# Kernel optimization log

Hardware: AMD Instinct MI355X
Metric: run time of the kernel (lower is better)

Reference implementation:

```python
import jax, jax.numpy as jnp
import numpy as np

ALPHA = 0.2  # LeakyReLU negative slope
NEG_BIG = -9e15

def setup_inputs() -> dict:
    key = jax.random.key(0)
    k1, k2, k3, k4 = jax.random.split(key, 4)
    B, N, Fin, Fout = 32, 1024, 64, 64
    x = jax.random.normal(k1, (B, N, Fin), dtype=jnp.float32)
    adj = jax.random.randint(k2, (B, N, N), 0, 2, dtype=jnp.int32)
    W = jax.random.normal(k3, (Fin, Fout), dtype=jnp.float32) * (1.414 / np.sqrt(Fin))
    a = jax.random.normal(k4, (2 * Fout, 1), dtype=jnp.float32) * 0.1
    return {"x": x, "adj": adj, "W": W, "a": a}

def reference(x, adj, W, a):
    # x: [B,N,Fin], adj: [B,N,N], W: [Fin,Fout], a: [2*Fout,1]
    h = jnp.einsum('bnf,fo->bno', x, W)               # [B,N,Fout]
    Fout = W.shape[1]
    a1 = a[:Fout, 0]                                   # source half
    a2 = a[Fout:, 0]                                   # target half
    # e_ij = leakyrelu(a1.h_i + a2.h_j)  (equivalent to concat+matmul)
    f = h @ a1                                         # [B,N]
    g = h @ a2                                         # [B,N]
    e = jax.nn.leaky_relu(f[:, :, None] + g[:, None, :], ALPHA)  # [B,N,N]
    att = jnp.where(adj > 0, e, jnp.float32(NEG_BIG))
    att = jax.nn.softmax(att, axis=2)                  # dropout p=0, eval mode
    h_prime = jnp.einsum('bij,bjo->bio', att, h)       # [B,N,Fout]
    return jax.nn.elu(h_prime)                         # concat=True -> elu
```

## Files before the change

### kernel.cpp

```cpp
#include <hip/hip_runtime.h>
#include <hip/hip_bf16.h>
#include <hip/hip_fp16.h>

#define NN 1024
#define FD 64
#define BB 32

typedef __attribute__((ext_vector_type(4))) float    f32x4;
typedef __attribute__((ext_vector_type(8))) _Float16 f16x8;

static __device__ __forceinline__ unsigned short f2hu(float x) {
  _Float16 h = (_Float16)x;
  return __builtin_bit_cast(unsigned short, h);
}

__global__ __launch_bounds__(256) void gat_k1(
    const float* __restrict__ x, const float* __restrict__ W,
    const float* __restrict__ av, float* __restrict__ fv,
    float* __restrict__ gv, unsigned short* __restrict__ hT)
{
  __shared__ __align__(16) float Wl[FD * FD];
  __shared__ __align__(16) float xl[FD * 68];
  __shared__ __align__(16) unsigned short tl[FD * FD];
  __shared__ __align__(16) float al[2 * FD];

  const int tid = threadIdx.x;
  const int b   = blockIdx.x >> 4;
  const int n0  = (blockIdx.x & 15) << 6;

  if (tid < 32) ((f32x4*)al)[tid] = ((const f32x4*)av)[tid];
  {
    const int r  = tid >> 2;
    const int cb = (tid & 3) << 2;
    const f32x4* Wg = (const f32x4*)W;
    const f32x4* xg = (const f32x4*)(x + ((size_t)(b * NN + n0)) * FD);
#pragma unroll
    for (int k = 0; k < 4; ++k) {
      f32x4 wv = Wg[r * 16 + cb + k];
      f32x4 xv = xg[r * 16 + cb + k];
      *(f32x4*)(Wl + r * FD + ((cb + k) << 2)) = wv;
      *(f32x4*)(xl + r * 68 + ((cb + k) << 2)) = xv;
    }
  }
  __syncthreads();

  const int r  = tid >> 2;
  const int o0 = (tid & 3) << 4;
  float acc[16];
#pragma unroll
  for (int i = 0; i < 16; ++i) acc[i] = 0.f;

#pragma unroll 8
  for (int f = 0; f < FD; ++f) {
    float xv = xl[r * 68 + f];
    const f32x4* wr = (const f32x4*)(Wl + f * FD + o0);
#pragma unroll
    for (int c = 0; c < 4; ++c) {
      f32x4 wv = wr[c];
      acc[c * 4 + 0] += xv * wv.x;
      acc[c * 4 + 1] += xv * wv.y;
      acc[c * 4 + 2] += xv * wv.z;
      acc[c * 4 + 3] += xv * wv.w;
    }
  }

  float fp = 0.f, gp = 0.f;
#pragma unroll
  for (int i = 0; i < 16; ++i) {
    fp += acc[i] * al[o0 + i];
    gp += acc[i] * al[FD + o0 + i];
  }
  fp += __shfl_xor(fp, 1); fp += __shfl_xor(fp, 2);
  gp += __shfl_xor(gp, 1); gp += __shfl_xor(gp, 2);
  if ((tid & 3) == 0) {
    fv[b * NN + n0 + r] = fp;
    gv[b * NN + n0 + r] = gp;
  }

#pragma unroll
  for (int i = 0; i < 16; ++i) {
    int o  = o0 + i;
    int sw = (o ^ (o >> 3)) & 7;
    tl[o * FD + ((((r >> 3) ^ sw) << 3) | (r & 7))] = f2hu(acc[i]);
  }
  __syncthreads();
  {
    const int c2 = tid & 7;
#pragma unroll
    for (int hh = 0; hh < 2; ++hh) {
      int o  = (tid >> 3) + 32 * hh;
      int sw = (o ^ (o >> 3)) & 7;
      f32x4 v = *(const f32x4*)(tl + o * FD + ((c2 ^ sw) << 3));
      *(f32x4*)(hT + ((size_t)(b * FD + o)) * NN + n0 + c2 * 8) = v;
    }
  }
}

__global__ __launch_bounds__(256) void gat_k2(
    const int* __restrict__ adj, const float* __restrict__ fv,
    const float* __restrict__ gv, const unsigned short* __restrict__ hT,
    float* __restrict__ out)
{
  __shared__ __align__(16) unsigned short Pl[2][32 * 64];
  __shared__ __align__(16) unsigned short Hl[2][64 * 64];
  __shared__ __align__(16) float gl[NN];
  __shared__ float dLds[32];
  __shared__ float red[8];

  const int tid  = threadIdx.x;
  const int b    = blockIdx.x >> 5;
  const int i0   = (blockIdx.x & 31) << 5;
  const int st   = blockIdx.x & 15;
  const int lane = tid & 63, w = tid >> 6;
  const int q = tid >> 3, s = tid & 7;
  const int bN = b * NN;

  f32x4 g4 = *(const f32x4*)(gv + bN + tid * 4);
  *(f32x4*)(gl + tid * 4) = g4;
  float gm = fmaxf(fmaxf(g4.x, g4.y), fmaxf(g4.z, g4.w));
  float fm = fv[bN + i0 + (tid & 31)];
#pragma unroll
  for (int m = 1; m < 64; m <<= 1) {
    gm = fmaxf(gm, __shfl_xor(gm, m));
    fm = fmaxf(fm, __shfl_xor(fm, m));
  }
  if (lane == 0) { red[w * 2] = gm; red[w * 2 + 1] = fm; }
  const float fr = fv[bN + i0 + q];
  __syncthreads();
  gm = fmaxf(fmaxf(red[0], red[2]), fmaxf(red[4], red[6]));
  fm = fmaxf(fmaxf(red[1], red[3]), fmaxf(red[5], red[7]));
  const float sm = fm + gm;
  const float Cb = fmaxf(sm, 0.2f * sm);

  const int*            adjS = adj + ((size_t)(bN + i0 + q)) * NN + s * 4;
  const unsigned short* hTS  = hT + ((size_t)(b * FD + q)) * NN + s * 8;

  float dAcc = 0.f;
  f32x4 acc[2];
  acc[0] = (f32x4){0.f, 0.f, 0.f, 0.f};
  acc[1] = (f32x4){0.f, 0.f, 0.f, 0.f};

  int4 Aa0, Aa1, Ah0, Ah1, Ba0, Ba1, Bh0, Bh1;

#define TLOAD(Ra0, Ra1, Rh0, Rh1, jt) do { const int j0_ = (jt) << 6; \
    Ra0 = *(const int4*)(adjS + j0_);                                 \
    Ra1 = *(const int4*)(adjS + j0_ + 32);                            \
    Rh0 = *(const int4*)(hTS + j0_);                                  \
    Rh1 = *(const int4*)(hTS + (size_t)32 * NN + j0_); } while (0)

#define PQUAD(avv, gg, half, p) do {                                       \
    float e0 = fr + gg.x; e0 = fmaxf(e0, 0.2f * e0) - Cb;                  \
    float e1 = fr + gg.y; e1 = fmaxf(e1, 0.2f * e1) - Cb;                  \
    float e2 = fr + gg.z; e2 = fmaxf(e2, 0.2f * e2) - Cb;                  \
    float e3 = fr + gg.w; e3 = fmaxf(e3, 0.2f * e3) - Cb;                  \
    float p0 = (avv.x > 0) ? __expf(e0) : 0.f;                             \
    float p1 = (avv.y > 0) ? __expf(e1) : 0.f;                             \
    float p2 = (avv.z > 0) ? __expf(e2) : 0.f;                             \
    float p3 = (avv.w > 0) ? __expf(e3) : 0.f;                             \
    dAcc += (p0 + p1) + (p2 + p3);                                         \
    uint2 uv_;                                                             \
    uv_.x = (unsigned)f2hu(p0) | ((unsigned)f2hu(p1) << 16);               \
    uv_.y = (unsigned)f2hu(p2) | ((unsigned)f2hu(p3) << 16);               \
    *(uint2*)(Pl[p] + q * 64 +                                             \
        (((((half) << 2) + (s >> 1)) ^ (q & 7)) << 3) + ((s & 1) << 2)) = uv_; \
  } while (0)

#define MSTEP(p) do {                                                      \
    const int m16_ = lane & 15, hi_ = lane >> 4;                           \
    const int ar_ = ((w & 1) << 4) + m16_;                                 \
    const f16x8 a0_ = *(const f16x8*)(Pl[p] + ar_ * 64 + (((hi_)     ^ (ar_ & 7)) << 3)); \
    const f16x8 a1_ = *(const f16x8*)(Pl[p] + ar_ * 64 + (((hi_ + 4) ^ (ar_ & 7)) << 3)); \
    _Pragma("unroll")                                                      \
    for (int n_ = 0; n_ < 2; ++n_) {                                       \
      const int o_ = ((w >> 1) << 5) + (n_ << 4) + m16_;                   \
      const f16x8 b0_ = *(const f16x8*)(Hl[p] + o_ * 64 + (((hi_)     ^ (o_ & 7)) << 3)); \
      const f16x8 b1_ = *(const f16x8*)(Hl[p] + o_ * 64 + (((hi_ + 4) ^ (o_ & 7)) << 3)); \
      acc[n_] = __builtin_amdgcn_mfma_f32_16x16x32_f16(a0_, b0_, acc[n_], 0, 0, 0);       \
      acc[n_] = __builtin_amdgcn_mfma_f32_16x16x32_f16(a1_, b1_, acc[n_], 0, 0, 0);       \
    }                                                                      \
  } while (0)

#define TILE_ONE(t, Ra0, Ra1, Rh0, Rh1, p) do {                            \
    const int jt_ = ((t) + st) & 15;                                       \
    const int jg_ = jt_ << 6;                                              \
    f32x4 g0_ = *(const f32x4*)(gl + jg_ + s * 4);                         \
    f32x4 g1_ = *(const f32x4*)(gl + jg_ + 32 + s * 4);                    \
    PQUAD(Ra0, g0_, 0, p); PQUAD(Ra1, g1_, 1, p);                          \
    *(int4*)(Hl[p] + q * 64 + ((s ^ (q & 7)) << 3)) = Rh0;                 \
    *(int4*)(Hl[p] + (q + 32) * 64 + ((s ^ (q & 7)) << 3)) = Rh1;          \
    if ((t) + 2 < 16) TLOAD(Ra0, Ra1, Rh0, Rh1, (((t) + 2 + st) & 15));    \
    asm volatile("s_waitcnt lgkmcnt(0)" ::: "memory");                     \
    __builtin_amdgcn_s_barrier();                                          \
    MSTEP(p);                                                              \
  } while (0)

  TLOAD(Aa0, Aa1, Ah0, Ah1, st);
  TLOAD(Ba0, Ba1, Bh0, Bh1, (st + 1) & 15);
#pragma unroll
  for (int t = 0; t < 16; t += 2) {
    TILE_ONE(t,     Aa0, Aa1, Ah0, Ah1, 0);
    TILE_ONE(t + 1, Ba0, Ba1, Bh0, Bh1, 1);
  }
#undef TLOAD
#undef PQUAD
#undef MSTEP
#undef TILE_ONE

  dAcc += __shfl_xor(dAcc, 1);
  dAcc += __shfl_xor(dAcc, 2);
  dAcc += __shfl_xor(dAcc, 4);
  if (s == 0) dLds[q] = dAcc;
  __syncthreads();

  const int m16 = lane & 15, hi4 = lane >> 4;
  const int wr = (w & 1) << 4, wc = (w >> 1) << 5;
  float* outp = out + ((size_t)(bN + i0 + wr + hi4 * 4)) * FD + wc + m16;
#pragma unroll
  for (int rr = 0; rr < 4; ++rr) {
    float d   = dLds[wr + hi4 * 4 + rr];
    float inv = d > 0.f ? 1.f / d : 0.f;
#pragma unroll
    for (int n = 0; n < 2; ++n) {
      float v = acc[n][rr] * inv;
      v = v > 0.f ? v : (__expf(v) - 1.f);
      outp[(size_t)rr * FD + n * 16] = v;
    }
  }
}

extern "C" void kernel_launch(void* const* d_in, const int* in_sizes, int n_in,
                              void* d_out, int out_size, void* d_ws, size_t ws_size,
                              hipStream_t stream) {
  const float* x   = (const float*)d_in[0];
  const int*   adj = (const int*)d_in[1];
  const float* W   = (const float*)d_in[2];
  const float* a   = (const float*)d_in[3];
  float* out = (float*)d_out;

  unsigned short* hT = (unsigned short*)d_ws;
  float* fv = (float*)((char*)d_ws + (size_t)BB * FD * NN * 2);
  float* gv = fv + (size_t)BB * NN;

  gat_k1<<<dim3(BB * 16), dim3(256), 0, stream>>>(x, W, a, fv, gv, hT);
  gat_k2<<<dim3(BB * 32), dim3(256), 0, stream>>>(adj, fv, gv, hT, out);
}
```

Measured before the change: 44.58 us.

## Precompute adjacency bitmask in first kernel and consume compact mask in attention kernel

Adds extra blocks to the first kernel that compress the int32 adjacency rows into 64-bit ballot bitmasks. The attention kernel then reads these small masks instead of 16-byte adjacency vectors per tile. This removes the heavy adj streaming from the MFMA loop and moves it into a pure bandwidth pass running alongside the projection. In exchange it adds a workspace round trip for the mask and an extra kernel dependency.

```diff
diff --git a/kernel.cpp b/kernel.cpp
--- a/kernel.cpp
+++ b/kernel.cpp
@@ -14,10 +14,11 @@
   return __builtin_bit_cast(unsigned short, h);
 }
 
-__global__ __launch_bounds__(256) void gat_k1(
+__global__ __launch_bounds__(256) void gat_k01(
     const float* __restrict__ x, const float* __restrict__ W,
-    const float* __restrict__ av, float* __restrict__ fv,
-    float* __restrict__ gv, unsigned short* __restrict__ hT)
+    const float* __restrict__ av, const int* __restrict__ adj,
+    float* __restrict__ fv, float* __restrict__ gv,
+    unsigned short* __restrict__ hT, unsigned long long* __restrict__ maskG)
 {
   __shared__ __align__(16) float Wl[FD * FD];
   __shared__ __align__(16) float xl[FD * 68];
@@ -25,79 +26,99 @@
   __shared__ __align__(16) float al[2 * FD];
 
   const int tid = threadIdx.x;
-  const int b   = blockIdx.x >> 4;
-  const int n0  = (blockIdx.x & 15) << 6;
-
-  if (tid < 32) ((f32x4*)al)[tid] = ((const f32x4*)av)[tid];
-  {
+  const int id  = blockIdx.x;
+
+  if (id < 512) {
+    const int b   = id >> 4;
+    const int n0  = (id & 15) << 6;
+
+    if (tid < 32) ((f32x4*)al)[tid] = ((const f32x4*)av)[tid];
+    {
+      const int r  = tid >> 2;
+      const int cb = (tid & 3) << 2;
+      const f32x4* Wg = (const f32x4*)W;
+      const f32x4* xg = (const f32x4*)(x + ((size_t)(b * NN + n0)) * FD);
+#pragma unroll
+      for (int k = 0; k < 4; ++k) {
+        f32x4 wv = Wg[r * 16 + cb + k];
+        f32x4 xv = xg[r * 16 + cb + k];
+        *(f32x4*)(Wl + r * FD + ((cb + k) << 2)) = wv;
+        *(f32x4*)(xl + r * 68 + ((cb + k) << 2)) = xv;
+      }
+    }
+    __syncthreads();
+
     const int r  = tid >> 2;
-    const int cb = (tid & 3) << 2;
-    const f32x4* Wg = (const f32x4*)W;
-    const f32x4* xg = (const f32x4*)(x + ((size_t)(b * NN + n0)) * FD);
-#pragma unroll
-    for (int k = 0; k < 4; ++k) {
-      f32x4 wv = Wg[r * 16 + cb + k];
-      f32x4 xv = xg[r * 16 + cb + k];
-      *(f32x4*)(Wl + r * FD + ((cb + k) << 2)) = wv;
-      *(f32x4*)(xl + r * 68 + ((cb + k) << 2)) = xv;
-    }
-  }
-  __syncthreads();
-
-  const int r  = tid >> 2;
-  const int o0 = (tid & 3) << 4;
-  float acc[16];
-#pragma unroll
-  for (int i = 0; i < 16; ++i) acc[i] = 0.f;
+    const int o0 = (tid & 3) << 4;
+    float acc[16];
+#pragma unroll
+    for (int i = 0; i < 16; ++i) acc[i] = 0.f;
 
 #pragma unroll 8
-  for (int f = 0; f < FD; ++f) {
-    float xv = xl[r * 68 + f];
-    const f32x4* wr = (const f32x4*)(Wl + f * FD + o0);
-#pragma unroll
-    for (int c = 0; c < 4; ++c) {
-      f32x4 wv = wr[c];
-      acc[c * 4 + 0] += xv * wv.x;
-      acc[c * 4 + 1] += xv * wv.y;
-      acc[c * 4 + 2] += xv * wv.z;
-      acc[c * 4 + 3] += xv * wv.w;
-    }
-  }
-
-  float fp = 0.f, gp = 0.f;
-#pragma unroll
-  for (int i = 0; i < 16; ++i) {
-    fp += acc[i] * al[o0 + i];
-    gp += acc[i] * al[FD + o0 + i];
-  }
-  fp += __shfl_xor(fp, 1); fp += __shfl_xor(fp, 2);
-  gp += __shfl_xor(gp, 1); gp += __shfl_xor(gp, 2);
-  if ((tid & 3) == 0) {
-    fv[b * NN + n0 + r] = fp;
-    gv[b * NN + n0 + r] = gp;
-  }
-
-#pragma unroll
-  for (int i = 0; i < 16; ++i) {
-    int o  = o0 + i;
-    int sw = (o ^ (o >> 3)) & 7;
-    tl[o * FD + ((((r >> 3) ^ sw) << 3) | (r & 7))] = f2hu(acc[i]);
-  }
-  __syncthreads();
-  {
-    const int c2 = tid & 7;
-#pragma unroll
-    for (int hh = 0; hh < 2; ++hh) {
-      int o  = (tid >> 3) + 32 * hh;
+    for (int f = 0; f < FD; ++f) {
+      float xv = xl[r * 68 + f];
+      const f32x4* wr = (const f32x4*)(Wl + f * FD + o0);
+#pragma unroll
+      for (int c = 0; c < 4; ++c) {
+        f32x4 wv = wr[c];
+        acc[c * 4 + 0] += xv * wv.x;
+        acc[c * 4 + 1] += xv * wv.y;
+        acc[c * 4 + 2] += xv * wv.z;
+        acc[c * 4 + 3] += xv * wv.w;
+      }
+    }
+
+    float fp = 0.f, gp = 0.f;
+#pragma unroll
+    for (int i = 0; i < 16; ++i) {
+      fp += acc[i] * al[o0 + i];
+      gp += acc[i] * al[FD + o0 + i];
+    }
+    fp += __shfl_xor(fp, 1); fp += __shfl_xor(fp, 2);
+    gp += __shfl_xor(gp, 1); gp += __shfl_xor(gp, 2);
+    if ((tid & 3) == 0) {
+      fv[b * NN + n0 + r] = fp;
+      gv[b * NN + n0 + r] = gp;
+    }
+
+#pragma unroll
+    for (int i = 0; i < 16; ++i) {
+      int o  = o0 + i;
       int sw = (o ^ (o >> 3)) & 7;
-      f32x4 v = *(const f32x4*)(tl + o * FD + ((c2 ^ sw) << 3));
-      *(f32x4*)(hT + ((size_t)(b * FD + o)) * NN + n0 + c2 * 8) = v;
+      tl[o * FD + ((((r >> 3) ^ sw) << 3) | (r & 7))] = f2hu(acc[i]);
+    }
+    __syncthreads();
+    {
+      const int c2 = tid & 7;
+#pragma unroll
+      for (int hh = 0; hh < 2; ++hh) {
+        int o  = (tid >> 3) + 32 * hh;
+        int sw = (o ^ (o >> 3)) & 7;
+        f32x4 v = *(const f32x4*)(tl + o * FD + ((c2 ^ sw) << 3));
+        *(f32x4*)(hT + ((size_t)(b * FD + o)) * NN + n0 + c2 * 8) = v;
+      }
+    }
+  } else {
+    const int cid = id - 512;
+    const int w = tid >> 6, l = tid & 63;
+    const int gw = cid * 4 + w;
+#pragma unroll
+    for (int rr = 0; rr < 4; ++rr) {
+      const int rowid = gw * 4 + rr;
+      const int* rp = adj + ((size_t)rowid << 10);
+      unsigned long long keep = 0ull;
+#pragma unroll
+      for (int t = 0; t < 16; ++t) {
+        unsigned long long bl = __ballot(rp[t * 64 + l] > 0);
+        if (l == t) keep = bl;
+      }
+      if (l < 16) maskG[((size_t)rowid << 4) + l] = keep;
     }
   }
 }
 
 __global__ __launch_bounds__(256) void gat_k2(
-    const int* __restrict__ adj, const float* __restrict__ fv,
+    const unsigned long long* __restrict__ maskG, const float* __restrict__ fv,
     const float* __restrict__ gv, const unsigned short* __restrict__ hT,
     float* __restrict__ out)
 {
@@ -132,31 +153,31 @@
   const float sm = fm + gm;
   const float Cb = fmaxf(sm, 0.2f * sm);
 
-  const int*            adjS = adj + ((size_t)(bN + i0 + q)) * NN + s * 4;
-  const unsigned short* hTS  = hT + ((size_t)(b * FD + q)) * NN + s * 8;
+  const unsigned long long* maskS = maskG + ((size_t)(bN + i0 + q) << 4);
+  const unsigned short*     hTS   = hT + ((size_t)(b * FD + q)) * NN + s * 8;
 
   float dAcc = 0.f;
   f32x4 acc[2];
   acc[0] = (f32x4){0.f, 0.f, 0.f, 0.f};
   acc[1] = (f32x4){0.f, 0.f, 0.f, 0.f};
 
-  int4 Aa0, Aa1, Ah0, Ah1, Ba0, Ba1, Bh0, Bh1;
-
-#define TLOAD(Ra0, Ra1, Rh0, Rh1, jt) do { const int j0_ = (jt) << 6; \
-    Ra0 = *(const int4*)(adjS + j0_);                                 \
-    Ra1 = *(const int4*)(adjS + j0_ + 32);                            \
-    Rh0 = *(const int4*)(hTS + j0_);                                  \
+  unsigned long long Am, Bm;
+  int4 Ah0, Ah1, Bh0, Bh1;
+
+#define TLOAD(Rm, Rh0, Rh1, jt) do { const int j0_ = (jt) << 6; \
+    Rm  = maskS[jt];                                            \
+    Rh0 = *(const int4*)(hTS + j0_);                            \
     Rh1 = *(const int4*)(hTS + (size_t)32 * NN + j0_); } while (0)
 
-#define PQUAD(avv, gg, half, p) do {                                       \
+#define PQUAD(nib, gg, half, p) do {                                       \
     float e0 = fr + gg.x; e0 = fmaxf(e0, 0.2f * e0) - Cb;                  \
     float e1 = fr + gg.y; e1 = fmaxf(e1, 0.2f * e1) - Cb;                  \
     float e2 = fr + gg.z; e2 = fmaxf(e2, 0.2f * e2) - Cb;                  \
     float e3 = fr + gg.w; e3 = fmaxf(e3, 0.2f * e3) - Cb;                  \
-    float p0 = (avv.x > 0) ? __expf(e0) : 0.f;                             \
-    float p1 = (avv.y > 0) ? __expf(e1) : 0.f;                             \
-    float p2 = (avv.z > 0) ? __expf(e2) : 0.f;                             \
-    float p3 = (avv.w > 0) ? __expf(e3) : 0.f;                             \
+    float p0 = (nib & 1u) ? __expf(e0) : 0.f;                              \
+    float p1 = (nib & 2u) ? __expf(e1) : 0.f;                              \
+    float p2 = (nib & 4u) ? __expf(e2) : 0.f;                              \
+    float p3 = (nib & 8u) ? __expf(e3) : 0.f;                              \
     dAcc += (p0 + p1) + (p2 + p3);                                         \
     uint2 uv_;                                                             \
     uv_.x = (unsigned)f2hu(p0) | ((unsigned)f2hu(p1) << 16);               \
@@ -180,26 +201,28 @@
     }                                                                      \
   } while (0)
 
-#define TILE_ONE(t, Ra0, Ra1, Rh0, Rh1, p) do {                            \
+#define TILE_ONE(t, Rm, Rh0, Rh1, p) do {                                  \
     const int jt_ = ((t) + st) & 15;                                       \
     const int jg_ = jt_ << 6;                                              \
     f32x4 g0_ = *(const f32x4*)(gl + jg_ + s * 4);                         \
     f32x4 g1_ = *(const f32x4*)(gl + jg_ + 32 + s * 4);                    \
-    PQUAD(Ra0, g0_, 0, p); PQUAD(Ra1, g1_, 1, p);                          \
+    unsigned na_ = (unsigned)(Rm >> (s * 4)) & 0xfu;                       \
+    unsigned nb_ = (unsigned)(Rm >> (32 + s * 4)) & 0xfu;                  \
+    PQUAD(na_, g0_, 0, p); PQUAD(nb_, g1_, 1, p);                          \
     *(int4*)(Hl[p] + q * 64 + ((s ^ (q & 7)) << 3)) = Rh0;                 \
     *(int4*)(Hl[p] + (q + 32) * 64 + ((s ^ (q & 7)) << 3)) = Rh1;          \
-    if ((t) + 2 < 16) TLOAD(Ra0, Ra1, Rh0, Rh1, (((t) + 2 + st) & 15));    \
+    if ((t) + 2 < 16) TLOAD(Rm, Rh0, Rh1, (((t) + 2 + st) & 15));          \
     asm volatile("s_waitcnt lgkmcnt(0)" ::: "memory");                     \
     __builtin_amdgcn_s_barrier();                                          \
     MSTEP(p);                                                              \
   } while (0)
 
-  TLOAD(Aa0, Aa1, Ah0, Ah1, st);
-  TLOAD(Ba0, Ba1, Bh0, Bh1, (st + 1) & 15);
+  TLOAD(Am, Ah0, Ah1, st);
+  TLOAD(Bm, Bh0, Bh1, (st + 1) & 15);
 #pragma unroll
   for (int t = 0; t < 16; t += 2) {
-    TILE_ONE(t,     Aa0, Aa1, Ah0, Ah1, 0);
-    TILE_ONE(t + 1, Ba0, Ba1, Bh0, Bh1, 1);
+    TILE_ONE(t,     Am, Ah0, Ah1, 0);
+    TILE_ONE(t + 1, Bm, Bh0, Bh1, 1);
   }
 #undef TLOAD
 #undef PQUAD
@@ -240,7 +263,8 @@
   unsigned short* hT = (unsigned short*)d_ws;
   float* fv = (float*)((char*)d_ws + (size_t)BB * FD * NN * 2);
   float* gv = fv + (size_t)BB * NN;
-
-  gat_k1<<<dim3(BB * 16), dim3(256), 0, stream>>>(x, W, a, fv, gv, hT);
-  gat_k2<<<dim3(BB * 32), dim3(256), 0, stream>>>(adj, fv, gv, hT, out);
-}
+  unsigned long long* maskG = (unsigned long long*)(gv + (size_t)BB * NN);
+
+  gat_k01<<<dim3(512 + 2048), dim3(256), 0, stream>>>(x, W, a, adj, fv, gv, hT, maskG);
+  gat_k2<<<dim3(BB * 32), dim3(256), 0, stream>>>(maskG, fv, gv, hT, out);
+}
```

Measured after the change: 47.41 us. 1.06x slower.
